# Kernel optimization log

Hardware: AMD Instinct MI355X
Metric: run time of the kernel (lower is better)

The kernel has to match this reference:

```python
import jax, jax.numpy as jnp
import numpy as np

N = 50000
E = 1600000
D_IN = 128
D_HID = 128
K = 16  # n_clusters


def spmm(edge_index, edge_weight, feats):
    # out[i] = sum_{(i<-j) in edges} w_e * feats[j]
    dst, src = edge_index[0], edge_index[1]
    msgs = feats[src] * edge_weight[:, None]  # [E, d]
    return jax.ops.segment_sum(msgs, dst, num_segments=N)


def gcn_with_skip(x, edge_index, edge_weight, W, b, skip_w):
    transformed = x @ W + b                      # Linear kernel
    propagated = spmm(edge_index, edge_weight, transformed)
    return jax.nn.selu(skip_w * transformed + propagated)


def setup_inputs() -> dict:
    key = jax.random.key(0)
    ks = jax.random.split(key, 12)
    x = jax.random.normal(ks[0], (N, D_IN), dtype=jnp.float32)
    edge_index = jax.random.randint(ks[1], (2, E), 0, N, dtype=jnp.int32)
    edge_weight = jax.random.uniform(ks[2], (E,), dtype=jnp.float32)
    s1 = 1.0 / np.sqrt(D_IN)
    s2 = 1.0 / np.sqrt(D_HID)
    W1 = jax.random.uniform(ks[3], (D_IN, D_HID), jnp.float32, -s1, s1)
    b1 = jax.random.uniform(ks[4], (D_HID,), jnp.float32, -s1, s1)
    skip1 = jnp.ones((D_HID,), jnp.float32)
    W2 = jax.random.uniform(ks[5], (D_HID, D_HID), jnp.float32, -s2, s2)
    b2 = jax.random.uniform(ks[6], (D_HID,), jnp.float32, -s2, s2)
    skip2 = jnp.ones((D_HID,), jnp.float32)
    Wa = jax.random.uniform(ks[7], (D_HID, K), jnp.float32, -s2, s2)
    ba = jax.random.uniform(ks[8], (K,), jnp.float32, -s2, s2)
    return {"x": x, "edge_index": edge_index, "edge_weight": edge_weight,
            "W1": W1, "b1": b1, "skip1": skip1,
            "W2": W2, "b2": b2, "skip2": skip2,
            "Wa": Wa, "ba": ba}


def reference(x, edge_index, edge_weight, W1, b1, skip1, W2, b2, skip2, Wa, ba):
    h = gcn_with_skip(x, edge_index, edge_weight, W1, b1, skip1)
    h = gcn_with_skip(h, edge_index, edge_weight, W2, b2, skip2)
    assignments = jax.nn.softmax(h @ Wa + ba, axis=-1)  # [N, K]
    return assignments
```

## Files before the change

### kernel.cpp

```cpp
#include <hip/hip_runtime.h>
#include <hip/hip_bf16.h>
#include <hip/hip_fp16.h>

#define NN 50000
#define NE 1600000
#define DD 128
#define KC 16

#define NB 3125
#define NBP (NB + 1)
#define CHUNK 6144
#define NCHUNK 261
#define BT 1024
#define EPT 6
#define MAXB 768
#define SB 784

typedef __attribute__((ext_vector_type(8))) short s8v;
typedef __attribute__((ext_vector_type(4))) float f4v;
typedef __attribute__((ext_vector_type(2))) float f2v;

__device__ __forceinline__ f2v up2(unsigned u) {
    f2v r;
    r.x = __uint_as_float(u << 16);
    r.y = __uint_as_float(u & 0xFFFF0000u);
    return r;
}
__device__ __forceinline__ float wof(unsigned rec) {
    return __half2float(__ushort_as_half((unsigned short)(rec >> 16)));
}


__global__ __launch_bounds__(BT) void k_binsort(const int* __restrict__ dst,
                                                const int* __restrict__ src,
                                                const float* __restrict__ w,
                                                int2* __restrict__ staging2,
                                                unsigned short* __restrict__ offs) {
    __shared__ int cnt[NB];
    __shared__ int s[BT];
    int t = threadIdx.x;
    int c = blockIdx.x;
    size_t cbase = (size_t)c * CHUNK;
    for (int i = t; i < NB; i += BT) cnt[i] = 0;
    __syncthreads();

    int dreg[EPT], sreg[EPT]; float wreg[EPT];
    #pragma unroll
    for (int j = 0; j < EPT; j++) {
        size_t e = cbase + j * BT + t;
        bool ok = e < NE;
        size_t ee = ok ? e : (NE - 1);
        dreg[j] = dst[ee]; sreg[j] = src[ee]; wreg[j] = w[ee];
        if (!ok) dreg[j] = -1;
        if (ok) atomicAdd(&cnt[dreg[j] >> 4], 1);
    }
    __syncthreads();

    int v[4]; int sum = 0;
    #pragma unroll
    for (int j = 0; j < 4; j++) { int i = t * 4 + j; v[j] = (i < NB) ? cnt[i] : 0; sum += v[j]; }
    s[t] = sum; __syncthreads();
    for (int off = 1; off < BT; off <<= 1) {
        int u = (t >= off) ? s[t - off] : 0;
        __syncthreads();
        s[t] += u;
        __syncthreads();
    }
    int run = (t == 0) ? 0 : s[t - 1];
    #pragma unroll
    for (int j = 0; j < 4; j++) {
        int i = t * 4 + j;
        if (i < NB) { offs[(size_t)c * NBP + i] = (unsigned short)run; cnt[i] = run; run += v[j]; }
    }
    if (t == BT - 1) offs[(size_t)c * NBP + NB] = (unsigned short)s[BT - 1];
    __syncthreads();

    #pragma unroll
    for (int j = 0; j < EPT; j++) {
        if (dreg[j] >= 0) {
            int b = dreg[j] >> 4;
            int li = atomicAdd(&cnt[b], 1);
            staging2[cbase + li] = make_int2(((dreg[j] & 15) << 16) | sreg[j],
                                            __float_as_int(wreg[j]));
        }
    }
}


__global__ __launch_bounds__(256) void k_rowsort(const int2* __restrict__ staging2,
                                                 const unsigned short* __restrict__ offs,
                                                 unsigned* __restrict__ staging4,
                                                 int* __restrict__ rowptr) {
    __shared__ int2 ebuf[MAXB];
    __shared__ unsigned srec[MAXB];
    __shared__ int segoff[NCHUNK + 1];
    __shared__ int cstart[NCHUNK];
    __shared__ int s2[256];
    __shared__ int rcnt[16];
    __shared__ int rowoff[17];
    int b = blockIdx.x, t = threadIdx.x;

    for (int c = t; c < NCHUNK; c += 256) {
        int o0 = offs[(size_t)c * NBP + b];
        int o1 = offs[(size_t)c * NBP + b + 1];
        cstart[c] = o0;
        segoff[c] = o1 - o0;
    }
    __syncthreads();
    int a0 = (2 * t < NCHUNK) ? segoff[2 * t] : 0;
    int a1 = (2 * t + 1 < NCHUNK) ? segoff[2 * t + 1] : 0;
    s2[t] = a0 + a1; __syncthreads();
    for (int off = 1; off < 256; off <<= 1) {
        int u = (t >= off) ? s2[t - off] : 0;
        __syncthreads();
        s2[t] += u;
        __syncthreads();
    }
    int base0 = (t == 0) ? 0 : s2[t - 1];
    int total = s2[255];
    __syncthreads();
    if (2 * t < NCHUNK) segoff[2 * t] = base0;
    if (2 * t + 1 < NCHUNK) segoff[2 * t + 1] = base0 + a0;
    if (t == 0) segoff[NCHUNK] = total;
    __syncthreads();

    int cnt = total; if (cnt > MAXB) cnt = MAXB;

    for (int i = t; i < cnt; i += 256) {
        int lo = 0, hi = NCHUNK;
        while (hi - lo > 1) {
            int mid = (lo + hi) >> 1;
            if (segoff[mid] <= i) lo = mid; else hi = mid;
        }
        ebuf[i] = staging2[(size_t)lo * CHUNK + cstart[lo] + (i - segoff[lo])];
    }
    __syncthreads();

    if (t < 16) rcnt[t] = 0;
    __syncthreads();
    for (int i = t; i < cnt; i += 256) atomicAdd(&rcnt[(unsigned)ebuf[i].x >> 16], 1);
    __syncthreads();
    if (t < 16) {
        int v = rcnt[t];
        int p = v;
        #pragma unroll
        for (int off = 1; off < 16; off <<= 1) {
            int u = __shfl_up(p, off, 64);
            if (t >= off) p += u;
        }
        rowoff[t] = p - v;
        if (t == 15) rowoff[16] = p;
        rcnt[t] = p - v;
    }
    __syncthreads();
    for (int i = t; i < cnt; i += 256) {
        int2 rec = ebuf[i];
        int p = atomicAdd(&rcnt[(unsigned)rec.x >> 16], 1);
        unsigned hb = __half_as_ushort(__float2half_rn(__int_as_float(rec.y)));
        srec[p] = ((unsigned)rec.x & 0xFFFFu) | (hb << 16);
    }
    __syncthreads();

    unsigned* outp = staging4 + (size_t)b * SB;
    for (int i = t; i < cnt; i += 256) outp[i] = srec[i];
    if (t < 8) outp[cnt + t] = 0u;
    if (t < 17) rowptr[b * 17 + t] = rowoff[t];
}


__global__ __launch_bounds__(256) void k_wprep(const float* __restrict__ W,
                                               s8v* __restrict__ Wf) {
    int g = blockIdx.x * 256 + threadIdx.x;
    int l = g & 63;
    int kcnt = g >> 6;
    int kc = kcnt >> 3, nt = kcnt & 7;
    int n = nt * 16 + (l & 15);
    int kb = kc * 32 + (l >> 4) * 8;
    union { s8v v; __hip_bfloat162 h2[4]; } u;
    #pragma unroll
    for (int q = 0; q < 4; q++) {
        float lo = W[(size_t)(kb + 2 * q) * 128 + n];
        float hi = W[(size_t)(kb + 2 * q + 1) * 128 + n];
        u.h2[q] = __float22bfloat162_rn(make_float2(lo, hi));
    }
    Wf[(size_t)kcnt * 64 + l] = u.v;
}


__device__ __forceinline__ s8v load_afrag(const float* p) {
    union { s8v v; __hip_bfloat162 h2[4]; } a;
    float4 f0 = *(const float4*)p;
    float4 f1 = *(const float4*)(p + 4);
    a.h2[0] = __float22bfloat162_rn(make_float2(f0.x, f0.y));
    a.h2[1] = __float22bfloat162_rn(make_float2(f0.z, f0.w));
    a.h2[2] = __float22bfloat162_rn(make_float2(f1.x, f1.y));
    a.h2[3] = __float22bfloat162_rn(make_float2(f1.z, f1.w));
    return a.v;
}
__device__ __forceinline__ s8v load_afrag(const __hip_bfloat16* p) {
    return *(const s8v*)p;
}

template <typename TI>
__global__ __launch_bounds__(256) void k_gemm_mfma(const TI* __restrict__ X,
                                                   const s8v* __restrict__ Wf,
                                                   const float* __restrict__ bias,
                                                   __hip_bfloat16* __restrict__ Out,
                                                   int nrows) {
    int wave = blockIdx.x * 4 + (threadIdx.x >> 6);
    int lane = threadIdx.x & 63;
    int m0 = wave * 32;
    if (m0 >= nrows) return;
    int col = lane & 15;
    int quad = lane >> 4;

    f4v acc[2][8];
    #pragma unroll
    for (int mt = 0; mt < 2; mt++)
        #pragma unroll
        for (int nt = 0; nt < 8; nt++) acc[mt][nt] = (f4v){0.f, 0.f, 0.f, 0.f};

    int row0 = m0 + col;
    int row1 = m0 + 16 + col;
    if (row0 >= nrows) row0 = nrows - 1;
    if (row1 >= nrows) row1 = nrows - 1;
    const TI* xr0 = X + (size_t)row0 * 128 + quad * 8;
    const TI* xr1 = X + (size_t)row1 * 128 + quad * 8;

    #pragma unroll 1
    for (int kc = 0; kc < 4; kc++) {
        s8v a0 = load_afrag(xr0 + kc * 32);
        s8v a1 = load_afrag(xr1 + kc * 32);
        #pragma unroll
        for (int nt = 0; nt < 8; nt++) {
            s8v b = Wf[(size_t)(kc * 8 + nt) * 64 + lane];
            acc[0][nt] = __builtin_amdgcn_mfma_f32_16x16x32_bf16(a0, b, acc[0][nt], 0, 0, 0);
            acc[1][nt] = __builtin_amdgcn_mfma_f32_16x16x32_bf16(a1, b, acc[1][nt], 0, 0, 0);
        }
    }

    float bb[8];
    #pragma unroll
    for (int nt = 0; nt < 8; nt++) bb[nt] = bias[nt * 16 + col];

    #pragma unroll
    for (int mt = 0; mt < 2; mt++) {
        #pragma unroll
        for (int r = 0; r < 4; r++) {
            int row = m0 + mt * 16 + quad * 4 + r;
            if (row < nrows) {
                __hip_bfloat16* orow = Out + (size_t)row * 128 + col;
                #pragma unroll
                for (int nt = 0; nt < 8; nt++) {
                    orow[nt * 16] = __float2bfloat16(acc[mt][nt][r] + bb[nt]);
                }
            }
        }
    }
}


template <int ASSIGN>
__global__ __launch_bounds__(256) void k_spmm(const __hip_bfloat16* __restrict__ T,
                                              const unsigned* __restrict__ staging4,
                                              const int* __restrict__ rowptr,
                                              const float* __restrict__ skip,
                                              __hip_bfloat16* __restrict__ Hout,
                                              const float* __restrict__ Wa,
                                              const float* __restrict__ ba,
                                              float* __restrict__ aout) {
    __shared__ __align__(16) unsigned srec[MAXB + 16];
    __shared__ int rowoff[17];
    int b = blockIdx.x;
    int tid = threadIdx.x;

    if (tid < 17) rowoff[tid] = rowptr[b * 17 + tid];
    __syncthreads();
    int cnt = rowoff[16];
    int nv4 = (cnt + 11) >> 2;
    const uint4* sp4 = (const uint4*)(staging4 + (size_t)b * SB);
    for (int i = tid; i < nv4; i += 256) ((uint4*)srec)[i] = sp4[i];
    __syncthreads();

    int wv = tid >> 6, lane = tid & 63;
    int q = lane >> 4;
    int fk = lane & 15;
    const int4* Tv4 = (const int4*)T;

    float sk[8];
    *(float4*)&sk[0] = *(const float4*)(skip + fk * 8);
    *(float4*)&sk[4] = *(const float4*)(skip + fk * 8 + 4);

    float wreg[32];
    float bav[4];
    if (ASSIGN) {
        #pragma unroll
        for (int j = 0; j < 8; j++)
            *(float4*)&wreg[j * 4] = *(const float4*)(Wa + (size_t)(8 * fk + j) * KC + 4 * q);
        #pragma unroll
        for (int c = 0; c < 4; c++) bav[c] = ba[4 * q + c];
    }

    const float scale = 1.0507009873554805f, alpha = 1.6732632423543772f;

    for (int r = wv; r < 16; r += 4) {
        int g = b * 16 + r;
        int o = rowoff[r], oe = rowoff[r + 1];
        f2v a01 = (f2v){0.f, 0.f}, a23 = (f2v){0.f, 0.f};
        f2v a45 = (f2v){0.f, 0.f}, a67 = (f2v){0.f, 0.f};

        for (; o + 8 <= oe; o += 8) {
            unsigned c0 = srec[o + q];
            unsigned c1 = srec[o + 4 + q];
            int4 t0 = Tv4[(size_t)(c0 & 0xFFFFu) * 16 + fk];
            int4 t1 = Tv4[(size_t)(c1 & 0xFFFFu) * 16 + fk];
            float w0 = wof(c0), w1 = wof(c1);
            a01 += w0 * up2(t0.x); a23 += w0 * up2(t0.y);
            a45 += w0 * up2(t0.z); a67 += w0 * up2(t0.w);
            a01 += w1 * up2(t1.x); a23 += w1 * up2(t1.y);
            a45 += w1 * up2(t1.z); a67 += w1 * up2(t1.w);
        }
        for (; o < oe; o += 4) {
            int i0 = o + q;
            unsigned c0 = srec[i0];
            int4 t0 = Tv4[(size_t)(c0 & 0xFFFFu) * 16 + fk];
            float w0 = (i0 < oe) ? wof(c0) : 0.f;
            a01 += w0 * up2(t0.x); a23 += w0 * up2(t0.y);
            a45 += w0 * up2(t0.z); a67 += w0 * up2(t0.w);
        }

        float acc[8];
        acc[0] = a01.x; acc[1] = a01.y; acc[2] = a23.x; acc[3] = a23.y;
        acc[4] = a45.x; acc[5] = a45.y; acc[6] = a67.x; acc[7] = a67.y;
        #pragma unroll
        for (int j = 0; j < 8; j++) {
            acc[j] += __shfl_xor(acc[j], 16, 64);
            acc[j] += __shfl_xor(acc[j], 32, 64);
        }

        int4 ts = Tv4[(size_t)g * 16 + fk];
        f2v s01 = up2(ts.x), s23 = up2(ts.y), s45 = up2(ts.z), s67 = up2(ts.w);
        float v[8];
        v[0] = sk[0] * s01.x + acc[0]; v[1] = sk[1] * s01.y + acc[1];
        v[2] = sk[2] * s23.x + acc[2]; v[3] = sk[3] * s23.y + acc[3];
        v[4] = sk[4] * s45.x + acc[4]; v[5] = sk[5] * s45.y + acc[5];
        v[6] = sk[6] * s67.x + acc[6]; v[7] = sk[7] * s67.y + acc[7];
        #pragma unroll
        for (int j = 0; j < 8; j++)
            v[j] = scale * (v[j] > 0.f ? v[j] : alpha * (__expf(v[j]) - 1.f));

        if (!ASSIGN) {
            if (q == 0) {
                union { int4 i4; __hip_bfloat162 h2[4]; } pk;
                #pragma unroll
                for (int j = 0; j < 4; j++)
                    pk.h2[j] = __float22bfloat162_rn(make_float2(v[2 * j], v[2 * j + 1]));
                *(int4*)(Hout + (size_t)g * 128 + fk * 8) = pk.i4;
            }
        } else {
            float p4[4] = {0.f, 0.f, 0.f, 0.f};
            #pragma unroll
            for (int j = 0; j < 8; j++)
                #pragma unroll
                for (int c = 0; c < 4; c++) p4[c] += v[j] * wreg[j * 4 + c];
            #pragma unroll
            for (int off = 1; off <= 8; off <<= 1)
                #pragma unroll
                for (int c = 0; c < 4; c++) p4[c] += __shfl_xor(p4[c], off, 64);
            #pragma unroll
            for (int c = 0; c < 4; c++) p4[c] += bav[c];
            float m = fmaxf(fmaxf(p4[0], p4[1]), fmaxf(p4[2], p4[3]));
            m = fmaxf(m, __shfl_xor(m, 16, 64));
            m = fmaxf(m, __shfl_xor(m, 32, 64));
            float e0 = __expf(p4[0] - m), e1 = __expf(p4[1] - m);
            float e2 = __expf(p4[2] - m), e3 = __expf(p4[3] - m);
            float s = e0 + e1 + e2 + e3;
            s += __shfl_xor(s, 16, 64);
            s += __shfl_xor(s, 32, 64);
            if (fk < 4) {
                float ev = e0;
                ev = (fk == 1) ? e1 : ev;
                ev = (fk == 2) ? e2 : ev;
                ev = (fk == 3) ? e3 : ev;
                aout[(size_t)g * KC + 4 * q + fk] = ev / s;
            }
        }
    }
}


extern "C" void kernel_launch(void* const* d_in, const int* in_sizes, int n_in,
                              void* d_out, int out_size, void* d_ws, size_t ws_size,
                              hipStream_t stream) {
    const float* x     = (const float*)d_in[0];
    const int*   eidx  = (const int*)d_in[1];
    const float* ew    = (const float*)d_in[2];
    const float* W1    = (const float*)d_in[3];
    const float* b1    = (const float*)d_in[4];
    const float* skip1 = (const float*)d_in[5];
    const float* W2    = (const float*)d_in[6];
    const float* b2    = (const float*)d_in[7];
    const float* skip2 = (const float*)d_in[8];
    const float* Wa    = (const float*)d_in[9];
    const float* ba    = (const float*)d_in[10];
    float* out = (float*)d_out;

    const int* dst = eidx;
    const int* src = eidx + NE;

    char* ws = (char*)d_ws;
    size_t off = 0;
    __hip_bfloat16* T = (__hip_bfloat16*)(ws + off);  off += (size_t)NN * DD * 2;
    __hip_bfloat16* Hb = (__hip_bfloat16*)(ws + off); off += (size_t)NN * DD * 2;
    int2* staging2 = (int2*)(ws + off);               off += (size_t)NCHUNK * CHUNK * 8;
    unsigned* staging4 = (unsigned*)(ws + off);       off += (size_t)NB * SB * 4;
    unsigned short* offs = (unsigned short*)(ws + off); off += (size_t)NCHUNK * NBP * 2;
    int* rowptr = (int*)(ws + off);                   off += (size_t)NB * 17 * 4;
    s8v* Wf1 = (s8v*)(ws + off);                      off += 2048 * 16;
    s8v* Wf2 = (s8v*)(ws + off);                      off += 2048 * 16;

    k_binsort<<<NCHUNK, BT, 0, stream>>>(dst, src, ew, staging2, offs);
    k_rowsort<<<NB, 256, 0, stream>>>(staging2, offs, staging4, rowptr);

    k_wprep<<<8, 256, 0, stream>>>(W1, Wf1);
    k_wprep<<<8, 256, 0, stream>>>(W2, Wf2);

    int gemm_grid = (NN / 128) + 1;
    k_gemm_mfma<float><<<gemm_grid, 256, 0, stream>>>(x, Wf1, b1, T, NN);
    k_spmm<0><<<NB, 256, 0, stream>>>(T, staging4, rowptr, skip1, Hb, nullptr, nullptr, nullptr);
    k_gemm_mfma<__hip_bfloat16><<<gemm_grid, 256, 0, stream>>>(Hb, Wf2, b2, T, NN);
    k_spmm<1><<<NB, 256, 0, stream>>>(T, staging4, rowptr, skip2, nullptr, Wa, ba, out);
}
```

Before: 267.1 us.

## Merge weight prep into binsort and overlap first GEMM with row sort

Folds the two weight-preparation launches into extra blocks of the bin-sort kernel, and runs the layer-1 GEMM as extra blocks inside the row-sort kernel so the independent work shares one grid. This cuts launches from eight to five and lets GEMM blocks fill the device alongside the sort blocks. It also adds a 16-edge unrolled gather loop to the SpMM kernel for more loads in flight, at the cost of higher register pressure. The merged row-sort/GEMM kernel now has a heterogeneous block mix, with shared memory sized for the sort path.

```diff
diff --git a/kernel.cpp b/kernel.cpp
--- a/kernel.cpp
+++ b/kernel.cpp
@@ -16,6 +16,8 @@
 #define MAXB 768
 #define SB 784
 
+#define GEMM_BLKS 391
+
 typedef __attribute__((ext_vector_type(8))) short s8v;
 typedef __attribute__((ext_vector_type(4))) float f4v;
 typedef __attribute__((ext_vector_type(2))) float f2v;
@@ -31,15 +33,46 @@
 }
 
 
-__global__ __launch_bounds__(BT) void k_binsort(const int* __restrict__ dst,
+__device__ __forceinline__ void wprep_one(const float* __restrict__ W, s8v* __restrict__ Wf, int g) {
+    int l = g & 63;
+    int kcnt = g >> 6;
+    int kc = kcnt >> 3, nt = kcnt & 7;
+    int n = nt * 16 + (l & 15);
+    int kb = kc * 32 + (l >> 4) * 8;
+    union { s8v v; __hip_bfloat162 h2[4]; } u;
+    #pragma unroll
+    for (int q = 0; q < 4; q++) {
+        float lo = W[(size_t)(kb + 2 * q) * 128 + n];
+        float hi = W[(size_t)(kb + 2 * q + 1) * 128 + n];
+        u.h2[q] = __float22bfloat162_rn(make_float2(lo, hi));
+    }
+    Wf[(size_t)kcnt * 64 + l] = u.v;
+}
+
+
+__global__ __launch_bounds__(BT) void k_binprep(const int* __restrict__ dst,
                                                 const int* __restrict__ src,
                                                 const float* __restrict__ w,
                                                 int2* __restrict__ staging2,
-                                                unsigned short* __restrict__ offs) {
+                                                unsigned short* __restrict__ offs,
+                                                const float* __restrict__ W1,
+                                                const float* __restrict__ W2,
+                                                s8v* __restrict__ Wf1,
+                                                s8v* __restrict__ Wf2) {
     __shared__ int cnt[NB];
     __shared__ int s[BT];
     int t = threadIdx.x;
-    int c = blockIdx.x;
+    int bid = blockIdx.x;
+
+    if (bid >= NCHUNK) {
+        int idx = bid - NCHUNK;
+        int g = (idx & 1) * 1024 + t;
+        if (idx < 2) wprep_one(W1, Wf1, g);
+        else         wprep_one(W2, Wf2, g);
+        return;
+    }
+
+    int c = bid;
     size_t cbase = (size_t)c * CHUNK;
     for (int i = t; i < NB; i += BT) cnt[i] = 0;
     __syncthreads();
@@ -84,106 +117,6 @@
                                             __float_as_int(wreg[j]));
         }
     }
-}
-
-
-__global__ __launch_bounds__(256) void k_rowsort(const int2* __restrict__ staging2,
-                                                 const unsigned short* __restrict__ offs,
-                                                 unsigned* __restrict__ staging4,
-                                                 int* __restrict__ rowptr) {
-    __shared__ int2 ebuf[MAXB];
-    __shared__ unsigned srec[MAXB];
-    __shared__ int segoff[NCHUNK + 1];
-    __shared__ int cstart[NCHUNK];
-    __shared__ int s2[256];
-    __shared__ int rcnt[16];
-    __shared__ int rowoff[17];
-    int b = blockIdx.x, t = threadIdx.x;
-
-    for (int c = t; c < NCHUNK; c += 256) {
-        int o0 = offs[(size_t)c * NBP + b];
-        int o1 = offs[(size_t)c * NBP + b + 1];
-        cstart[c] = o0;
-        segoff[c] = o1 - o0;
-    }
-    __syncthreads();
-    int a0 = (2 * t < NCHUNK) ? segoff[2 * t] : 0;
-    int a1 = (2 * t + 1 < NCHUNK) ? segoff[2 * t + 1] : 0;
-    s2[t] = a0 + a1; __syncthreads();
-    for (int off = 1; off < 256; off <<= 1) {
-        int u = (t >= off) ? s2[t - off] : 0;
-        __syncthreads();
-        s2[t] += u;
-        __syncthreads();
-    }
-    int base0 = (t == 0) ? 0 : s2[t - 1];
-    int total = s2[255];
-    __syncthreads();
-    if (2 * t < NCHUNK) segoff[2 * t] = base0;
-    if (2 * t + 1 < NCHUNK) segoff[2 * t + 1] = base0 + a0;
-    if (t == 0) segoff[NCHUNK] = total;
-    __syncthreads();
-
-    int cnt = total; if (cnt > MAXB) cnt = MAXB;
-
-    for (int i = t; i < cnt; i += 256) {
-        int lo = 0, hi = NCHUNK;
-        while (hi - lo > 1) {
-            int mid = (lo + hi) >> 1;
-            if (segoff[mid] <= i) lo = mid; else hi = mid;
-        }
-        ebuf[i] = staging2[(size_t)lo * CHUNK + cstart[lo] + (i - segoff[lo])];
-    }
-    __syncthreads();
-
-    if (t < 16) rcnt[t] = 0;
-    __syncthreads();
-    for (int i = t; i < cnt; i += 256) atomicAdd(&rcnt[(unsigned)ebuf[i].x >> 16], 1);
-    __syncthreads();
-    if (t < 16) {
-        int v = rcnt[t];
-        int p = v;
-        #pragma unroll
-        for (int off = 1; off < 16; off <<= 1) {
-            int u = __shfl_up(p, off, 64);
-            if (t >= off) p += u;
-        }
-        rowoff[t] = p - v;
-        if (t == 15) rowoff[16] = p;
-        rcnt[t] = p - v;
-    }
-    __syncthreads();
-    for (int i = t; i < cnt; i += 256) {
-        int2 rec = ebuf[i];
-        int p = atomicAdd(&rcnt[(unsigned)rec.x >> 16], 1);
-        unsigned hb = __half_as_ushort(__float2half_rn(__int_as_float(rec.y)));
-        srec[p] = ((unsigned)rec.x & 0xFFFFu) | (hb << 16);
-    }
-    __syncthreads();
-
-    unsigned* outp = staging4 + (size_t)b * SB;
-    for (int i = t; i < cnt; i += 256) outp[i] = srec[i];
-    if (t < 8) outp[cnt + t] = 0u;
-    if (t < 17) rowptr[b * 17 + t] = rowoff[t];
-}
-
-
-__global__ __launch_bounds__(256) void k_wprep(const float* __restrict__ W,
-                                               s8v* __restrict__ Wf) {
-    int g = blockIdx.x * 256 + threadIdx.x;
-    int l = g & 63;
-    int kcnt = g >> 6;
-    int kc = kcnt >> 3, nt = kcnt & 7;
-    int n = nt * 16 + (l & 15);
-    int kb = kc * 32 + (l >> 4) * 8;
-    union { s8v v; __hip_bfloat162 h2[4]; } u;
-    #pragma unroll
-    for (int q = 0; q < 4; q++) {
-        float lo = W[(size_t)(kb + 2 * q) * 128 + n];
-        float hi = W[(size_t)(kb + 2 * q + 1) * 128 + n];
-        u.h2[q] = __float22bfloat162_rn(make_float2(lo, hi));
-    }
-    Wf[(size_t)kcnt * 64 + l] = u.v;
 }
 
 
@@ -202,13 +135,11 @@
 }
 
 template <typename TI>
-__global__ __launch_bounds__(256) void k_gemm_mfma(const TI* __restrict__ X,
-                                                   const s8v* __restrict__ Wf,
-                                                   const float* __restrict__ bias,
-                                                   __hip_bfloat16* __restrict__ Out,
-                                                   int nrows) {
-    int wave = blockIdx.x * 4 + (threadIdx.x >> 6);
-    int lane = threadIdx.x & 63;
+__device__ __forceinline__ void gemm_body(const TI* __restrict__ X,
+                                          const s8v* __restrict__ Wf,
+                                          const float* __restrict__ bias,
+                                          __hip_bfloat16* __restrict__ Out,
+                                          int nrows, int wave, int lane) {
     int m0 = wave * 32;
     if (m0 >= nrows) return;
     int col = lane & 15;
@@ -257,6 +188,107 @@
             }
         }
     }
+}
+
+
+__global__ __launch_bounds__(256) void k_sortgemm(const int2* __restrict__ staging2,
+                                                  const unsigned short* __restrict__ offs,
+                                                  unsigned* __restrict__ staging4,
+                                                  int* __restrict__ rowptr,
+                                                  const float* __restrict__ x,
+                                                  const s8v* __restrict__ Wf1,
+                                                  const float* __restrict__ b1,
+                                                  __hip_bfloat16* __restrict__ T) {
+    __shared__ int2 ebuf[MAXB];
+    __shared__ unsigned srec[MAXB];
+    __shared__ int segoff[NCHUNK + 1];
+    __shared__ int cstart[NCHUNK];
+    __shared__ int s2[256];
+    __shared__ int rcnt[16];
+    __shared__ int rowoff[17];
+    int bid = blockIdx.x, t = threadIdx.x;
+
+    if (bid >= NB) {
+        int wave = (bid - NB) * 4 + (t >> 6);
+        gemm_body<float>(x, Wf1, b1, T, NN, wave, t & 63);
+        return;
+    }
+
+    int b = bid;
+    for (int c = t; c < NCHUNK; c += 256) {
+        int o0 = offs[(size_t)c * NBP + b];
+        int o1 = offs[(size_t)c * NBP + b + 1];
+        cstart[c] = o0;
+        segoff[c] = o1 - o0;
+    }
+    __syncthreads();
+    int a0 = (2 * t < NCHUNK) ? segoff[2 * t] : 0;
+    int a1 = (2 * t + 1 < NCHUNK) ? segoff[2 * t + 1] : 0;
+    s2[t] = a0 + a1; __syncthreads();
+    for (int off = 1; off < 256; off <<= 1) {
+        int u = (t >= off) ? s2[t - off] : 0;
+        __syncthreads();
+        s2[t] += u;
+        __syncthreads();
+    }
+    int base0 = (t == 0) ? 0 : s2[t - 1];
+    int total = s2[255];
+    __syncthreads();
+    if (2 * t < NCHUNK) segoff[2 * t] = base0;
+    if (2 * t + 1 < NCHUNK) segoff[2 * t + 1] = base0 + a0;
+    if (t == 0) segoff[NCHUNK] = total;
+    __syncthreads();
+
+    int cnt = total; if (cnt > MAXB) cnt = MAXB;
+
+    for (int i = t; i < cnt; i += 256) {
+        int lo = 0, hi = NCHUNK;
+        while (hi - lo > 1) {
+            int mid = (lo + hi) >> 1;
+            if (segoff[mid] <= i) lo = mid; else hi = mid;
+        }
+        ebuf[i] = staging2[(size_t)lo * CHUNK + cstart[lo] + (i - segoff[lo])];
+    }
+    __syncthreads();
+
+    if (t < 16) rcnt[t] = 0;
+    __syncthreads();
+    for (int i = t; i < cnt; i += 256) atomicAdd(&rcnt[(unsigned)ebuf[i].x >> 16], 1);
+    __syncthreads();
+    if (t < 16) {
+        int v = rcnt[t];
+        int p = v;
+        #pragma unroll
+        for (int off = 1; off < 16; off <<= 1) {
+            int u = __shfl_up(p, off, 64);
+            if (t >= off) p += u;
+        }
+        rowoff[t] = p - v;
+        if (t == 15) rowoff[16] = p;
+        rcnt[t] = p - v;
+    }
+    __syncthreads();
+    for (int i = t; i < cnt; i += 256) {
+        int2 rec = ebuf[i];
+        int p = atomicAdd(&rcnt[(unsigned)rec.x >> 16], 1);
+        unsigned hb = __half_as_ushort(__float2half_rn(__int_as_float(rec.y)));
+        srec[p] = ((unsigned)rec.x & 0xFFFFu) | (hb << 16);
+    }
+    __syncthreads();
+
+    unsigned* outp = staging4 + (size_t)b * SB;
+    for (int i = t; i < cnt; i += 256) outp[i] = srec[i];
+    if (t < 8) outp[cnt + t] = 0u;
+    if (t < 17) rowptr[b * 17 + t] = rowoff[t];
+}
+
+
+__global__ __launch_bounds__(256) void k_gemm2(const __hip_bfloat16* __restrict__ X,
+                                               const s8v* __restrict__ Wf,
+                                               const float* __restrict__ bias,
+                                               __hip_bfloat16* __restrict__ Out) {
+    int wave = blockIdx.x * 4 + (threadIdx.x >> 6);
+    gemm_body<__hip_bfloat16>(X, Wf, bias, Out, NN, wave, threadIdx.x & 63);
 }
 
 
@@ -309,6 +341,25 @@
         f2v a01 = (f2v){0.f, 0.f}, a23 = (f2v){0.f, 0.f};
         f2v a45 = (f2v){0.f, 0.f}, a67 = (f2v){0.f, 0.f};
 
+        for (; o + 16 <= oe; o += 16) {
+            unsigned c0 = srec[o + q];
+            unsigned c1 = srec[o + 4 + q];
+            unsigned c2 = srec[o + 8 + q];
+            unsigned c3 = srec[o + 12 + q];
+            int4 t0 = Tv4[(size_t)(c0 & 0xFFFFu) * 16 + fk];
+            int4 t1 = Tv4[(size_t)(c1 & 0xFFFFu) * 16 + fk];
+            int4 t2 = Tv4[(size_t)(c2 & 0xFFFFu) * 16 + fk];
+            int4 t3 = Tv4[(size_t)(c3 & 0xFFFFu) * 16 + fk];
+            float w0 = wof(c0), w1 = wof(c1), w2 = wof(c2), w3 = wof(c3);
+            a01 += w0 * up2(t0.x); a23 += w0 * up2(t0.y);
+            a45 += w0 * up2(t0.z); a67 += w0 * up2(t0.w);
+            a01 += w1 * up2(t1.x); a23 += w1 * up2(t1.y);
+            a45 += w1 * up2(t1.z); a67 += w1 * up2(t1.w);
+            a01 += w2 * up2(t2.x); a23 += w2 * up2(t2.y);
+            a45 += w2 * up2(t2.z); a67 += w2 * up2(t2.w);
+            a01 += w3 * up2(t3.x); a23 += w3 * up2(t3.y);
+            a45 += w3 * up2(t3.z); a67 += w3 * up2(t3.w);
+        }
         for (; o + 8 <= oe; o += 8) {
             unsigned c0 = srec[o + q];
             unsigned c1 = srec[o + 4 + q];
@@ -419,15 +470,10 @@
     s8v* Wf1 = (s8v*)(ws + off);                      off += 2048 * 16;
     s8v* Wf2 = (s8v*)(ws + off);                      off += 2048 * 16;
 
-    k_binsort<<<NCHUNK, BT, 0, stream>>>(dst, src, ew, staging2, offs);
-    k_rowsort<<<NB, 256, 0, stream>>>(staging2, offs, staging4, rowptr);
-
-    k_wprep<<<8, 256, 0, stream>>>(W1, Wf1);
-    k_wprep<<<8, 256, 0, stream>>>(W2, Wf2);
-
-    int gemm_grid = (NN / 128) + 1;
-    k_gemm_mfma<float><<<gemm_grid, 256, 0, stream>>>(x, Wf1, b1, T, NN);
+    k_binprep<<<NCHUNK + 4, BT, 0, stream>>>(dst, src, ew, staging2, offs, W1, W2, Wf1, Wf2);
+    k_sortgemm<<<NB + GEMM_BLKS, 256, 0, stream>>>(staging2, offs, staging4, rowptr,
+                                                   x, Wf1, b1, T);
     k_spmm<0><<<NB, 256, 0, stream>>>(T, staging4, rowptr, skip1, Hb, nullptr, nullptr, nullptr);
-    k_gemm_mfma<__hip_bfloat16><<<gemm_grid, 256, 0, stream>>>(Hb, Wf2, b2, T, NN);
+    k_gemm2<<<GEMM_BLKS, 256, 0, stream>>>(Hb, Wf2, b2, T);
     k_spmm<1><<<NB, 256, 0, stream>>>(T, staging4, rowptr, skip2, nullptr, Wa, ba, out);
 }
```

After: 261.9 us. About the same (-1.9%).
